# Kernel optimization log

Measured on AMD Instinct MI355X. Metric: run time of the kernel, lower is better.

## Reference

```python
import jax, jax.numpy as jnp
import numpy as np

N = 30000        # nodes
E = 480000       # edges (before self-loops)
F_IN = 512       # input feature dim
HID = 64         # per-head hidden dim
HEADS = 4
WIDTH = HID * HEADS  # 256, concat heads
LAYERS = 3
NCLS = 40
NEG_SLOPE = 0.2


def setup_inputs() -> dict:
    key = jax.random.key(0)
    ks = jax.random.split(key, 16)
    def p(k, shape, scale=0.1):
        return jax.random.normal(k, shape, dtype=jnp.float32) * scale
    return {
        "x": jax.random.normal(ks[0], (N, F_IN), dtype=jnp.float32),
        "edge_index": jax.random.randint(ks[1], (2, E), 0, N, dtype=jnp.int32),
        # layer 1: F_IN -> HEADS*HID (concat)
        "W1": p(ks[2], (F_IN, WIDTH)), "as1": p(ks[3], (HEADS, HID)), "ad1": p(ks[4], (HEADS, HID)), "b1": p(ks[5], (WIDTH,)),
        # layer 2: WIDTH -> WIDTH
        "W2": p(ks[6], (WIDTH, WIDTH)), "as2": p(ks[7], (HEADS, HID)), "ad2": p(ks[8], (HEADS, HID)), "b2": p(ks[9], (WIDTH,)),
        # layer 3: WIDTH -> WIDTH
        "W3": p(ks[10], (WIDTH, WIDTH)), "as3": p(ks[11], (HEADS, HID)), "ad3": p(ks[12], (HEADS, HID)), "b3": p(ks[13], (WIDTH,)),
        # JK='cat' output head: WIDTH*LAYERS -> NCLS
        "Wo": p(ks[14], (WIDTH * LAYERS, NCLS)), "bo": p(ks[15], (NCLS,)),
    }


def gat_layer(x, Wm, a_src, a_dst, b, src, dst):
    # PyG GATConv (concat=True, eval mode): h = xW reshaped [N,H,C];
    # e_ij = leaky_relu(a_src.h_j + a_dst.h_i) for edge j->i, softmax over dst groups.
    n = x.shape[0]
    H, C = a_src.shape
    h = (x @ Wm).reshape(n, H, C)                      # [N,H,C]
    es = jnp.sum(h * a_src, axis=-1)                   # [N,H]
    ed = jnp.sum(h * a_dst, axis=-1)                   # [N,H]
    e = jax.nn.leaky_relu(es[src] + ed[dst], NEG_SLOPE)  # [Etot,H]
    m = jax.ops.segment_max(e, dst, num_segments=n)    # stable softmax per dst node
    w = jnp.exp(e - m[dst])
    den = jax.ops.segment_sum(w, dst, num_segments=n)
    alpha = w / den[dst]                               # [Etot,H]
    out = jax.ops.segment_sum(h[src] * alpha[:, :, None], dst, num_segments=n)  # [N,H,C]
    return out.reshape(n, H * C) + b


def reference(x, edge_index, W1, as1, ad1, b1, W2, as2, ad2, b2, W3, as3, ad3, b3, Wo, bo):
    # add self-loops (PyG GATConv default)
    loops = jnp.arange(N, dtype=edge_index.dtype)
    src = jnp.concatenate([edge_index[0], loops])
    dst = jnp.concatenate([edge_index[1], loops])
    # dropout is identity in eval mode
    h1 = jax.nn.relu(gat_layer(x, W1, as1, ad1, b1, src, dst))
    h2 = jax.nn.relu(gat_layer(h1, W2, as2, ad2, b2, src, dst))
    h3 = jax.nn.relu(gat_layer(h2, W3, as3, ad3, b3, src, dst))
    h = jnp.concatenate([h1, h2, h3], axis=-1)         # JK 'cat': [N, WIDTH*LAYERS]
    return h @ Wo + bo                                 # [N, NCLS]
```

## Files before the change

### kernel.cpp

```cpp
#include <hip/hip_runtime.h>

#define N_NODES 30000
#define N_EDGES 480000
#define ETOT    510000
#define F_IN    512
#define WIDTH   256
#define NCLS    40
#define KCAT    768
#define NPAD    48

typedef __attribute__((ext_vector_type(8))) short short8;
typedef __attribute__((ext_vector_type(4))) float f32x4;

__device__ __forceinline__ unsigned short f2bf(float f){
  unsigned u = __float_as_uint(f);
  u += 0x7fffu + ((u >> 16) & 1u);
  return (unsigned short)(u >> 16);
}
__device__ __forceinline__ float b2f(unsigned short s){
  return __uint_as_float(((unsigned)s) << 16);
}

__global__ void cast4_kernel(const float* __restrict__ in, unsigned short* __restrict__ out, int n4){
  int i = blockIdx.x * blockDim.x + threadIdx.x;
  if (i < n4){
    float4 v = *(const float4*)(in + 4*(size_t)i);
    ushort4 o;
    o.x = f2bf(v.x); o.y = f2bf(v.y); o.z = f2bf(v.z); o.w = f2bf(v.w);
    *(ushort4*)(out + 4*(size_t)i) = o;
  }
}

__global__ void transpose_w_kernel(const float* __restrict__ W, unsigned short* __restrict__ Wt,
                                   int K, int Nc){
  int k = blockIdx.x * blockDim.x + threadIdx.x;
  int n = blockIdx.y;
  if (k < K) Wt[(size_t)n * K + k] = f2bf(W[(size_t)k * Nc + n]);
}

__global__ void transpose_wo_kernel(const float* __restrict__ Wo, unsigned short* __restrict__ WoT){
  int i = blockIdx.x * blockDim.x + threadIdx.x;
  if (i < NPAD * KCAT){
    int c = i / KCAT, k = i - c * KCAT;
    WoT[i] = (c < NCLS) ? f2bf(Wo[(size_t)k * NCLS + c]) : (unsigned short)0;
  }
}

__global__ void zero_kernel(int* __restrict__ p, int n){
  int i = blockIdx.x * blockDim.x + threadIdx.x;
  if (i < n) p[i] = 0;
}

__global__ void hist_kernel(const int* __restrict__ ei, int* __restrict__ counts){
  int e = blockIdx.x * blockDim.x + threadIdx.x;
  if (e < ETOT){
    int d = (e < N_EDGES) ? ei[N_EDGES + e] : (e - N_EDGES);
    atomicAdd(&counts[d], 1);
  }
}

__global__ __launch_bounds__(1024) void scan_kernel(const int* __restrict__ counts,
                                                    int* __restrict__ offsets,
                                                    int* __restrict__ cursor, int n){
  __shared__ int wsum[16];
  int tid = threadIdx.x, lane = tid & 63, wid = tid >> 6;
  int running = 0;
  int nchunks = (n + 1023) >> 10;
  for (int ch = 0; ch < nchunks; ++ch){
    int i = (ch << 10) + tid;
    int v = (i < n) ? counts[i] : 0;
    int x = v;
    #pragma unroll
    for (int off = 1; off < 64; off <<= 1){
      int t = __shfl_up(x, off, 64);
      if (lane >= off) x += t;
    }
    if (lane == 63) wsum[wid] = x;
    __syncthreads();
    if (wid == 0){
      int s = (lane < 16) ? wsum[lane] : 0;
      #pragma unroll
      for (int off = 1; off < 16; off <<= 1){
        int t = __shfl_up(s, off, 64);
        if (lane >= off) s += t;
      }
      if (lane < 16) wsum[lane] = s;
    }
    __syncthreads();
    int waveprefix = (wid > 0) ? wsum[wid - 1] : 0;
    int excl = x - v + waveprefix + running;
    if (i < n){ offsets[i] = excl; cursor[i] = excl; }
    running += wsum[15];
    __syncthreads();
  }
  if (tid == 0) offsets[n] = running;
}

__global__ void scatter_kernel(const int* __restrict__ ei, int* __restrict__ cursor,
                               int* __restrict__ srcs){
  int e = blockIdx.x * blockDim.x + threadIdx.x;
  if (e < ETOT){
    int s, d;
    if (e < N_EDGES){ s = ei[e]; d = ei[N_EDGES + e]; }
    else { s = e - N_EDGES; d = s; }
    int pos = atomicAdd(&cursor[d], 1);
    srcs[pos] = s;
  }
}

#define BM 64
#define BK 32
#define LDA 40

__global__ __launch_bounds__(256) void gemm_bf16_kernel(const unsigned short* __restrict__ A,
                                                        const unsigned short* __restrict__ Bt,
                                                        float* __restrict__ C,
                                                        int M, int K){
  __shared__ unsigned short Als[BM * LDA];
  __shared__ unsigned short Bls[256 * LDA];
  int tid = threadIdx.x;
  int lane = tid & 63, wid = tid >> 6;
  int l15 = lane & 15, quad = lane >> 4;
  int m0 = blockIdx.x * BM;

  f32x4 acc[16];
  #pragma unroll
  for (int t = 0; t < 16; ++t) acc[t] = (f32x4){0.f, 0.f, 0.f, 0.f};

  for (int k0 = 0; k0 < K; k0 += BK){
    __syncthreads();
    {
      int row = tid >> 2, g = tid & 3;
      int grow = m0 + row; if (grow >= M) grow = M - 1;
      uint4 av = *(const uint4*)(A + (size_t)grow * K + k0 + 8 * g);
      *(uint4*)(&Als[row * LDA + 8 * g]) = av;
      const unsigned short* src = Bt + (size_t)tid * K + k0;
      uint4 b0 = *(const uint4*)(src);
      uint4 b1 = *(const uint4*)(src + 8);
      uint4 b2 = *(const uint4*)(src + 16);
      uint4 b3 = *(const uint4*)(src + 24);
      unsigned short* dst = &Bls[tid * LDA];
      *(uint4*)(dst) = b0;
      *(uint4*)(dst + 8) = b1;
      *(uint4*)(dst + 16) = b2;
      *(uint4*)(dst + 24) = b3;
    }
    __syncthreads();
    short8 af = *(const short8*)(&Als[(16 * wid + l15) * LDA + quad * 8]);
    #pragma unroll
    for (int t = 0; t < 16; ++t){
      short8 bf = *(const short8*)(&Bls[(16 * t + l15) * LDA + quad * 8]);
      acc[t] = __builtin_amdgcn_mfma_f32_16x16x32_bf16(af, bf, acc[t], 0, 0, 0);
    }
  }

  int row0 = m0 + 16 * wid + quad * 4;
  #pragma unroll
  for (int t = 0; t < 16; ++t){
    int col = 16 * t + l15;
    #pragma unroll
    for (int r = 0; r < 4; ++r){
      int grow = row0 + r;
      if (grow < M) C[(size_t)grow * WIDTH + col] = acc[t][r];
    }
  }
}

__global__ __launch_bounds__(256) void esed_kernel(const float* __restrict__ hpre,
                                                   const float* __restrict__ a_s,
                                                   const float* __restrict__ a_d,
                                                   float* __restrict__ es, float* __restrict__ ed,
                                                   unsigned short* __restrict__ hb){
  int n = blockIdx.x * 4 + (threadIdx.x >> 6);
  int lane = threadIdx.x & 63;
  float4 h = *(const float4*)(hpre + (size_t)n * WIDTH + 4 * lane);
  int head = lane >> 4, cl = (lane & 15) * 4;
  float4 as = *(const float4*)(a_s + head * 64 + cl);
  float4 ad = *(const float4*)(a_d + head * 64 + cl);
  float ps = h.x * as.x + h.y * as.y + h.z * as.z + h.w * as.w;
  float pd = h.x * ad.x + h.y * ad.y + h.z * ad.z + h.w * ad.w;
  #pragma unroll
  for (int off = 1; off < 16; off <<= 1){
    ps += __shfl_xor(ps, off, 64);
    pd += __shfl_xor(pd, off, 64);
  }
  if ((lane & 15) == 0){
    es[n * 4 + head] = ps;
    ed[n * 4 + head] = pd;
  }
  ushort4 o;
  o.x = f2bf(h.x); o.y = f2bf(h.y); o.z = f2bf(h.z); o.w = f2bf(h.w);
  *(ushort4*)(hb + (size_t)n * WIDTH + 4 * lane) = o;
}

__global__ __launch_bounds__(256) void agg_kernel(const int* __restrict__ offsets,
                                                  const int* __restrict__ srcs,
                                                  const float* __restrict__ es,
                                                  const float* __restrict__ ed,
                                                  const unsigned short* __restrict__ hb,
                                                  const float* __restrict__ bias,
                                                  unsigned short* __restrict__ hout){
  __shared__ float eLds[4][64][4];
  int wid = threadIdx.x >> 6;
  int n = blockIdx.x * 4 + wid;
  int lane = threadIdx.x & 63;
  int half = lane >> 5, l32 = lane & 31;
  int base = offsets[n];
  int deg = offsets[n + 1] - base;
  float4 edv = *(const float4*)(ed + n * 4);

  float m0 = -1e30f, m1 = -1e30f, m2 = -1e30f, m3 = -1e30f;
  for (int i = lane; i < deg; i += 64){
    int s = srcs[base + i];
    float4 ev = *(const float4*)(es + s * 4);
    float e0 = ev.x + edv.x, e1 = ev.y + edv.y, e2 = ev.z + edv.z, e3 = ev.w + edv.w;
    e0 = e0 > 0.f ? e0 : 0.2f * e0;
    e1 = e1 > 0.f ? e1 : 0.2f * e1;
    e2 = e2 > 0.f ? e2 : 0.2f * e2;
    e3 = e3 > 0.f ? e3 : 0.2f * e3;
    if (i < 64) *(float4*)(&eLds[wid][i][0]) = (float4){e0, e1, e2, e3};
    m0 = fmaxf(m0, e0); m1 = fmaxf(m1, e1); m2 = fmaxf(m2, e2); m3 = fmaxf(m3, e3);
  }
  #pragma unroll
  for (int off = 32; off; off >>= 1){
    m0 = fmaxf(m0, __shfl_xor(m0, off, 64));
    m1 = fmaxf(m1, __shfl_xor(m1, off, 64));
    m2 = fmaxf(m2, __shfl_xor(m2, off, 64));
    m3 = fmaxf(m3, __shfl_xor(m3, off, 64));
  }
  int head = l32 >> 3;
  float mh  = (head == 0) ? m0 : (head == 1) ? m1 : (head == 2) ? m2 : m3;
  float edh = (head == 0) ? edv.x : (head == 1) ? edv.y : (head == 2) ? edv.z : edv.w;

  float a0=0.f,a1=0.f,a2=0.f,a3=0.f,a4=0.f,a5=0.f,a6=0.f,a7=0.f;
  float den = 0.f;
  const unsigned short* hcol = hb + 8 * l32;
  for (int i = 0; i < deg; i += 8){
    int sidx[4]; float w[4];
    #pragma unroll
    for (int u = 0; u < 4; ++u){
      int idx = i + 2 * u + half;
      bool v = idx < deg;
      sidx[u] = srcs[base + (v ? idx : 0)];
      float le;
      if (idx < 64){
        le = eLds[wid][v ? idx : 0][head];
      } else {
        float e = es[sidx[u] * 4 + head] + edh;
        le = e > 0.f ? e : 0.2f * e;
      }
      w[u] = v ? __expf(le - mh) : 0.f;
    }
    uint4 hv[4];
    #pragma unroll
    for (int u = 0; u < 4; ++u)
      hv[u] = *(const uint4*)(hcol + (size_t)sidx[u] * WIDTH);
    #pragma unroll
    for (int u = 0; u < 4; ++u){
      float wu = w[u];
      den += wu;
      a0 += wu * b2f((unsigned short)(hv[u].x & 0xffff));
      a1 += wu * b2f((unsigned short)(hv[u].x >> 16));
      a2 += wu * b2f((unsigned short)(hv[u].y & 0xffff));
      a3 += wu * b2f((unsigned short)(hv[u].y >> 16));
      a4 += wu * b2f((unsigned short)(hv[u].z & 0xffff));
      a5 += wu * b2f((unsigned short)(hv[u].z >> 16));
      a6 += wu * b2f((unsigned short)(hv[u].w & 0xffff));
      a7 += wu * b2f((unsigned short)(hv[u].w >> 16));
    }
  }
  den += __shfl_xor(den, 32, 64);
  a0 += __shfl_xor(a0, 32, 64); a1 += __shfl_xor(a1, 32, 64);
  a2 += __shfl_xor(a2, 32, 64); a3 += __shfl_xor(a3, 32, 64);
  a4 += __shfl_xor(a4, 32, 64); a5 += __shfl_xor(a5, 32, 64);
  a6 += __shfl_xor(a6, 32, 64); a7 += __shfl_xor(a7, 32, 64);

  if (half == 0){
    float inv = 1.0f / den;
    const float* bp = bias + 8 * l32;
    float4 bv0 = *(const float4*)(bp);
    float4 bv1 = *(const float4*)(bp + 4);
    float o0 = fmaxf(a0 * inv + bv0.x, 0.f);
    float o1 = fmaxf(a1 * inv + bv0.y, 0.f);
    float o2 = fmaxf(a2 * inv + bv0.z, 0.f);
    float o3 = fmaxf(a3 * inv + bv0.w, 0.f);
    float o4 = fmaxf(a4 * inv + bv1.x, 0.f);
    float o5 = fmaxf(a5 * inv + bv1.y, 0.f);
    float o6 = fmaxf(a6 * inv + bv1.z, 0.f);
    float o7 = fmaxf(a7 * inv + bv1.w, 0.f);
    uint4 o;
    o.x = (unsigned)f2bf(o0) | ((unsigned)f2bf(o1) << 16);
    o.y = (unsigned)f2bf(o2) | ((unsigned)f2bf(o3) << 16);
    o.z = (unsigned)f2bf(o4) | ((unsigned)f2bf(o5) << 16);
    o.w = (unsigned)f2bf(o6) | ((unsigned)f2bf(o7) << 16);
    *(uint4*)(hout + (size_t)n * WIDTH + 8 * l32) = o;
  }
}

__global__ __launch_bounds__(256) void out_gemm_kernel(const unsigned short* __restrict__ h1,
                                                       const unsigned short* __restrict__ h2,
                                                       const unsigned short* __restrict__ h3,
                                                       const unsigned short* __restrict__ WoT,
                                                       const float* __restrict__ bo,
                                                       float* __restrict__ out){
  int tid = threadIdx.x, lane = tid & 63, wid = tid >> 6;
  int l15 = lane & 15, quad = lane >> 4;
  int m0 = blockIdx.x * 64 + 16 * wid;

  f32x4 acc[3];
  #pragma unroll
  for (int t = 0; t < 3; ++t) acc[t] = (f32x4){0.f, 0.f, 0.f, 0.f};

  int arow = m0 + l15; if (arow >= N_NODES) arow = N_NODES - 1;

  #pragma unroll
  for (int part = 0; part < 3; ++part){
    const unsigned short* hp = (part == 0) ? h1 : (part == 1) ? h2 : h3;
    const unsigned short* ap = hp + (size_t)arow * WIDTH;
    #pragma unroll
    for (int k0 = 0; k0 < WIDTH; k0 += 32){
      short8 af = *(const short8*)(ap + k0 + quad * 8);
      int kk = part * WIDTH + k0;
      #pragma unroll
      for (int t = 0; t < 3; ++t){
        short8 bf = *(const short8*)(WoT + (size_t)(16 * t + l15) * KCAT + kk + quad * 8);
        acc[t] = __builtin_amdgcn_mfma_f32_16x16x32_bf16(af, bf, acc[t], 0, 0, 0);
      }
    }
  }

  int r0 = m0 + quad * 4;
  #pragma unroll
  for (int t = 0; t < 3; ++t){
    int col = 16 * t + l15;
    if (col < NCLS){
      float bc = bo[col];
      #pragma unroll
      for (int r = 0; r < 4; ++r){
        int grow = r0 + r;
        if (grow < N_NODES) out[(size_t)grow * NCLS + col] = acc[t][r] + bc;
      }
    }
  }
}

static inline size_t align256(size_t x){ return (x + 255) & ~(size_t)255; }

extern "C" void kernel_launch(void* const* d_in, const int* in_sizes, int n_in,
                              void* d_out, int out_size, void* d_ws, size_t ws_size,
                              hipStream_t stream) {
  const float* x   = (const float*)d_in[0];
  const int*   ei  = (const int*)  d_in[1];
  const float* W1  = (const float*)d_in[2];
  const float* as1 = (const float*)d_in[3];
  const float* ad1 = (const float*)d_in[4];
  const float* b1  = (const float*)d_in[5];
  const float* W2  = (const float*)d_in[6];
  const float* as2 = (const float*)d_in[7];
  const float* ad2 = (const float*)d_in[8];
  const float* b2  = (const float*)d_in[9];
  const float* W3  = (const float*)d_in[10];
  const float* as3 = (const float*)d_in[11];
  const float* ad3 = (const float*)d_in[12];
  const float* b3  = (const float*)d_in[13];
  const float* Wo  = (const float*)d_in[14];
  const float* bo  = (const float*)d_in[15];
  float* out = (float*)d_out;

  char* p = (char*)d_ws;
  auto take = [&](size_t bytes) -> char* { char* cur = p; p += align256(bytes); return cur; };

  unsigned short* xb    = (unsigned short*)take((size_t)N_NODES * F_IN * 2);
  unsigned short* Wt1   = (unsigned short*)take((size_t)WIDTH * F_IN * 2);
  unsigned short* Wt2   = (unsigned short*)take((size_t)WIDTH * WIDTH * 2);
  unsigned short* Wt3   = (unsigned short*)take((size_t)WIDTH * WIDTH * 2);
  unsigned short* WoT   = (unsigned short*)take((size_t)NPAD * KCAT * 2);
  float*          hpre  = (float*)take((size_t)N_NODES * WIDTH * 4);
  unsigned short* hpreb = (unsigned short*)take((size_t)N_NODES * WIDTH * 2);
  float*          es    = (float*)take((size_t)N_NODES * 4 * 4);
  float*          ed    = (float*)take((size_t)N_NODES * 4 * 4);
  unsigned short* h1b   = (unsigned short*)take((size_t)N_NODES * WIDTH * 2);
  unsigned short* h2b   = (unsigned short*)take((size_t)N_NODES * WIDTH * 2);
  unsigned short* h3b   = (unsigned short*)take((size_t)N_NODES * WIDTH * 2);
  int*            counts  = (int*)take((size_t)N_NODES * 4);
  int*            offsets = (int*)take((size_t)(N_NODES + 1) * 4);
  int*            cursor  = (int*)take((size_t)N_NODES * 4);
  int*            srcs    = (int*)take((size_t)ETOT * 4);

  cast4_kernel<<<(N_NODES * F_IN / 4 + 255) / 256, 256, 0, stream>>>(x, xb, N_NODES * F_IN / 4);
  transpose_w_kernel<<<dim3(F_IN / 256, WIDTH), 256, 0, stream>>>(W1, Wt1, F_IN, WIDTH);
  transpose_w_kernel<<<dim3(1, WIDTH), 256, 0, stream>>>(W2, Wt2, WIDTH, WIDTH);
  transpose_w_kernel<<<dim3(1, WIDTH), 256, 0, stream>>>(W3, Wt3, WIDTH, WIDTH);
  transpose_wo_kernel<<<(NPAD * KCAT + 255) / 256, 256, 0, stream>>>(Wo, WoT);

  zero_kernel<<<(N_NODES + 255) / 256, 256, 0, stream>>>(counts, N_NODES);
  hist_kernel<<<(ETOT + 255) / 256, 256, 0, stream>>>(ei, counts);
  scan_kernel<<<1, 1024, 0, stream>>>(counts, offsets, cursor, N_NODES);
  scatter_kernel<<<(ETOT + 255) / 256, 256, 0, stream>>>(ei, cursor, srcs);

  const int gemm_grid = (N_NODES + BM - 1) / BM;
  const int node_grid = N_NODES / 4;

  gemm_bf16_kernel<<<gemm_grid, 256, 0, stream>>>(xb, Wt1, hpre, N_NODES, F_IN);
  esed_kernel<<<node_grid, 256, 0, stream>>>(hpre, as1, ad1, es, ed, hpreb);
  agg_kernel<<<node_grid, 256, 0, stream>>>(offsets, srcs, es, ed, hpreb, b1, h1b);
  gemm_bf16_kernel<<<gemm_grid, 256, 0, stream>>>(h1b, Wt2, hpre, N_NODES, WIDTH);
  esed_kernel<<<node_grid, 256, 0, stream>>>(hpre, as2, ad2, es, ed, hpreb);
  agg_kernel<<<node_grid, 256, 0, stream>>>(offsets, srcs, es, ed, hpreb, b2, h2b);
  gemm_bf16_kernel<<<gemm_grid, 256, 0, stream>>>(h2b, Wt3, hpre, N_NODES, WIDTH);
  esed_kernel<<<node_grid, 256, 0, stream>>>(hpre, as3, ad3, es, ed, hpreb);
  agg_kernel<<<node_grid, 256, 0, stream>>>(offsets, srcs, es, ed, hpreb, b3, h3b);

  out_gemm_kernel<<<gemm_grid, 256, 0, stream>>>(h1b, h2b, h3b, WoT, bo, out);
}
```

Measured before the change: 435.5 us.

## Fuse cast and attention-score epilogue into GEMM; one node per half-wave in aggregation

The layer-1 GEMM now reads fp32 x and converts it to bf16 while loading tiles, which removes the separate cast kernel and the bf16 copy of x. Each GEMM epilogue writes bf16 h directly and computes the es/ed attention dot products from the accumulators with shuffles, which removes the fp32 hpre buffer and the esed kernel. The aggregation kernel assigns one node per 32-lane half-wave instead of splitting a node across two halves, caches source indices in LDS, and unrolls the gather to 8 edges. The trade-off is an extra cross-lane reduction in the GEMM epilogue, plus less parallelism per high-degree node and more register pressure in the aggregation loop.

```diff
diff --git a/kernel.cpp b/kernel.cpp
--- a/kernel.cpp
+++ b/kernel.cpp
@@ -19,16 +19,6 @@
 }
 __device__ __forceinline__ float b2f(unsigned short s){
   return __uint_as_float(((unsigned)s) << 16);
-}
-
-__global__ void cast4_kernel(const float* __restrict__ in, unsigned short* __restrict__ out, int n4){
-  int i = blockIdx.x * blockDim.x + threadIdx.x;
-  if (i < n4){
-    float4 v = *(const float4*)(in + 4*(size_t)i);
-    ushort4 o;
-    o.x = f2bf(v.x); o.y = f2bf(v.y); o.z = f2bf(v.z); o.w = f2bf(v.w);
-    *(ushort4*)(out + 4*(size_t)i) = o;
-  }
 }
 
 __global__ void transpose_w_kernel(const float* __restrict__ W, unsigned short* __restrict__ Wt,
@@ -112,10 +102,15 @@
 #define BK 32
 #define LDA 40
 
-__global__ __launch_bounds__(256) void gemm_bf16_kernel(const unsigned short* __restrict__ A,
-                                                        const unsigned short* __restrict__ Bt,
-                                                        float* __restrict__ C,
-                                                        int M, int K){
+template<bool AF32>
+__global__ __launch_bounds__(256) void gemm_fused_kernel(const void* __restrict__ Araw,
+                                                         const unsigned short* __restrict__ Bt,
+                                                         const float* __restrict__ a_s,
+                                                         const float* __restrict__ a_d,
+                                                         float* __restrict__ es,
+                                                         float* __restrict__ ed,
+                                                         unsigned short* __restrict__ hb,
+                                                         int M, int K){
   __shared__ unsigned short Als[BM * LDA];
   __shared__ unsigned short Bls[256 * LDA];
   int tid = threadIdx.x;
@@ -132,8 +127,19 @@
     {
       int row = tid >> 2, g = tid & 3;
       int grow = m0 + row; if (grow >= M) grow = M - 1;
-      uint4 av = *(const uint4*)(A + (size_t)grow * K + k0 + 8 * g);
-      *(uint4*)(&Als[row * LDA + 8 * g]) = av;
+      if (AF32){
+        const float* Af = (const float*)Araw + (size_t)grow * K + k0 + 8 * g;
+        float4 v0 = *(const float4*)(Af);
+        float4 v1 = *(const float4*)(Af + 4);
+        ushort4 p0 = {f2bf(v0.x), f2bf(v0.y), f2bf(v0.z), f2bf(v0.w)};
+        ushort4 p1 = {f2bf(v1.x), f2bf(v1.y), f2bf(v1.z), f2bf(v1.w)};
+        *(ushort4*)(&Als[row * LDA + 8 * g])     = p0;
+        *(ushort4*)(&Als[row * LDA + 8 * g + 4]) = p1;
+      } else {
+        const unsigned short* Ab = (const unsigned short*)Araw;
+        uint4 av = *(const uint4*)(Ab + (size_t)grow * K + k0 + 8 * g);
+        *(uint4*)(&Als[row * LDA + 8 * g]) = av;
+      }
       const unsigned short* src = Bt + (size_t)tid * K + k0;
       uint4 b0 = *(const uint4*)(src);
       uint4 b1 = *(const uint4*)(src + 8);
@@ -155,42 +161,47 @@
   }
 
   int row0 = m0 + 16 * wid + quad * 4;
+
   #pragma unroll
   for (int t = 0; t < 16; ++t){
     int col = 16 * t + l15;
     #pragma unroll
     for (int r = 0; r < 4; ++r){
       int grow = row0 + r;
-      if (grow < M) C[(size_t)grow * WIDTH + col] = acc[t][r];
-    }
-  }
-}
-
-__global__ __launch_bounds__(256) void esed_kernel(const float* __restrict__ hpre,
-                                                   const float* __restrict__ a_s,
-                                                   const float* __restrict__ a_d,
-                                                   float* __restrict__ es, float* __restrict__ ed,
-                                                   unsigned short* __restrict__ hb){
-  int n = blockIdx.x * 4 + (threadIdx.x >> 6);
-  int lane = threadIdx.x & 63;
-  float4 h = *(const float4*)(hpre + (size_t)n * WIDTH + 4 * lane);
-  int head = lane >> 4, cl = (lane & 15) * 4;
-  float4 as = *(const float4*)(a_s + head * 64 + cl);
-  float4 ad = *(const float4*)(a_d + head * 64 + cl);
-  float ps = h.x * as.x + h.y * as.y + h.z * as.z + h.w * as.w;
-  float pd = h.x * ad.x + h.y * ad.y + h.z * ad.z + h.w * ad.w;
-  #pragma unroll
-  for (int off = 1; off < 16; off <<= 1){
-    ps += __shfl_xor(ps, off, 64);
-    pd += __shfl_xor(pd, off, 64);
-  }
-  if ((lane & 15) == 0){
-    es[n * 4 + head] = ps;
-    ed[n * 4 + head] = pd;
-  }
-  ushort4 o;
-  o.x = f2bf(h.x); o.y = f2bf(h.y); o.z = f2bf(h.z); o.w = f2bf(h.w);
-  *(ushort4*)(hb + (size_t)n * WIDTH + 4 * lane) = o;
+      if (grow < M) hb[(size_t)grow * WIDTH + col] = f2bf(acc[t][r]);
+    }
+  }
+
+  float as_v[16], ad_v[16];
+  #pragma unroll
+  for (int t = 0; t < 16; ++t){
+    int cc = 16 * (t & 3) + l15;
+    as_v[t] = a_s[(t >> 2) * 64 + cc];
+    ad_v[t] = a_d[(t >> 2) * 64 + cc];
+  }
+  #pragma unroll
+  for (int h = 0; h < 4; ++h){
+    #pragma unroll
+    for (int r = 0; r < 4; ++r){
+      float se = 0.f, sd = 0.f;
+      #pragma unroll
+      for (int tt = 0; tt < 4; ++tt){
+        int t = 4 * h + tt;
+        se += acc[t][r] * as_v[t];
+        sd += acc[t][r] * ad_v[t];
+      }
+      #pragma unroll
+      for (int off = 1; off < 16; off <<= 1){
+        se += __shfl_xor(se, off, 64);
+        sd += __shfl_xor(sd, off, 64);
+      }
+      int grow = row0 + r;
+      if (l15 == 0 && grow < M){
+        es[grow * 4 + h] = se;
+        ed[grow * 4 + h] = sd;
+      }
+    }
+  }
 }
 
 __global__ __launch_bounds__(256) void agg_kernel(const int* __restrict__ offsets,
@@ -200,17 +211,19 @@
                                                   const unsigned short* __restrict__ hb,
                                                   const float* __restrict__ bias,
                                                   unsigned short* __restrict__ hout){
-  __shared__ float eLds[4][64][4];
+  __shared__ float eLds[8][64][4];
+  __shared__ int   sLds[8][64];
   int wid = threadIdx.x >> 6;
-  int n = blockIdx.x * 4 + wid;
   int lane = threadIdx.x & 63;
   int half = lane >> 5, l32 = lane & 31;
+  int slot = wid * 2 + half;
+  int n = blockIdx.x * 8 + slot;
   int base = offsets[n];
   int deg = offsets[n + 1] - base;
   float4 edv = *(const float4*)(ed + n * 4);
 
   float m0 = -1e30f, m1 = -1e30f, m2 = -1e30f, m3 = -1e30f;
-  for (int i = lane; i < deg; i += 64){
+  for (int i = l32; i < deg; i += 32){
     int s = srcs[base + i];
     float4 ev = *(const float4*)(es + s * 4);
     float e0 = ev.x + edv.x, e1 = ev.y + edv.y, e2 = ev.z + edv.z, e3 = ev.w + edv.w;
@@ -218,11 +231,14 @@
     e1 = e1 > 0.f ? e1 : 0.2f * e1;
     e2 = e2 > 0.f ? e2 : 0.2f * e2;
     e3 = e3 > 0.f ? e3 : 0.2f * e3;
-    if (i < 64) *(float4*)(&eLds[wid][i][0]) = (float4){e0, e1, e2, e3};
+    if (i < 64){
+      sLds[slot][i] = s;
+      *(float4*)(&eLds[slot][i][0]) = (float4){e0, e1, e2, e3};
+    }
     m0 = fmaxf(m0, e0); m1 = fmaxf(m1, e1); m2 = fmaxf(m2, e2); m3 = fmaxf(m3, e3);
   }
   #pragma unroll
-  for (int off = 32; off; off >>= 1){
+  for (int off = 1; off < 32; off <<= 1){
     m0 = fmaxf(m0, __shfl_xor(m0, off, 64));
     m1 = fmaxf(m1, __shfl_xor(m1, off, 64));
     m2 = fmaxf(m2, __shfl_xor(m2, off, 64));
@@ -232,69 +248,65 @@
   float mh  = (head == 0) ? m0 : (head == 1) ? m1 : (head == 2) ? m2 : m3;
   float edh = (head == 0) ? edv.x : (head == 1) ? edv.y : (head == 2) ? edv.z : edv.w;
 
-  float a0=0.f,a1=0.f,a2=0.f,a3=0.f,a4=0.f,a5=0.f,a6=0.f,a7=0.f;
+  float2 a0 = {0.f,0.f}, a1 = {0.f,0.f}, a2 = {0.f,0.f}, a3 = {0.f,0.f};
   float den = 0.f;
   const unsigned short* hcol = hb + 8 * l32;
   for (int i = 0; i < deg; i += 8){
-    int sidx[4]; float w[4];
-    #pragma unroll
-    for (int u = 0; u < 4; ++u){
-      int idx = i + 2 * u + half;
+    int sidx[8]; float w[8];
+    #pragma unroll
+    for (int u = 0; u < 8; ++u){
+      int idx = i + u;
       bool v = idx < deg;
-      sidx[u] = srcs[base + (v ? idx : 0)];
-      float le;
-      if (idx < 64){
-        le = eLds[wid][v ? idx : 0][head];
+      float le; int s;
+      if (idx < 64 || !v){
+        int ic = v ? idx : 0;
+        if (ic >= 64) ic = 0;
+        s  = sLds[slot][ic];
+        le = eLds[slot][ic][head];
       } else {
-        float e = es[sidx[u] * 4 + head] + edh;
+        s = srcs[base + idx];
+        float e = es[s * 4 + head] + edh;
         le = e > 0.f ? e : 0.2f * e;
       }
+      sidx[u] = s;
       w[u] = v ? __expf(le - mh) : 0.f;
     }
-    uint4 hv[4];
-    #pragma unroll
-    for (int u = 0; u < 4; ++u)
+    uint4 hv[8];
+    #pragma unroll
+    for (int u = 0; u < 8; ++u)
       hv[u] = *(const uint4*)(hcol + (size_t)sidx[u] * WIDTH);
     #pragma unroll
-    for (int u = 0; u < 4; ++u){
+    for (int u = 0; u < 8; ++u){
       float wu = w[u];
       den += wu;
-      a0 += wu * b2f((unsigned short)(hv[u].x & 0xffff));
-      a1 += wu * b2f((unsigned short)(hv[u].x >> 16));
-      a2 += wu * b2f((unsigned short)(hv[u].y & 0xffff));
-      a3 += wu * b2f((unsigned short)(hv[u].y >> 16));
-      a4 += wu * b2f((unsigned short)(hv[u].z & 0xffff));
-      a5 += wu * b2f((unsigned short)(hv[u].z >> 16));
-      a6 += wu * b2f((unsigned short)(hv[u].w & 0xffff));
-      a7 += wu * b2f((unsigned short)(hv[u].w >> 16));
-    }
-  }
-  den += __shfl_xor(den, 32, 64);
-  a0 += __shfl_xor(a0, 32, 64); a1 += __shfl_xor(a1, 32, 64);
-  a2 += __shfl_xor(a2, 32, 64); a3 += __shfl_xor(a3, 32, 64);
-  a4 += __shfl_xor(a4, 32, 64); a5 += __shfl_xor(a5, 32, 64);
-  a6 += __shfl_xor(a6, 32, 64); a7 += __shfl_xor(a7, 32, 64);
-
-  if (half == 0){
-    float inv = 1.0f / den;
-    const float* bp = bias + 8 * l32;
-    float4 bv0 = *(const float4*)(bp);
-    float4 bv1 = *(const float4*)(bp + 4);
-    float o0 = fmaxf(a0 * inv + bv0.x, 0.f);
-    float o1 = fmaxf(a1 * inv + bv0.y, 0.f);
-    float o2 = fmaxf(a2 * inv + bv0.z, 0.f);
-    float o3 = fmaxf(a3 * inv + bv0.w, 0.f);
-    float o4 = fmaxf(a4 * inv + bv1.x, 0.f);
-    float o5 = fmaxf(a5 * inv + bv1.y, 0.f);
-    float o6 = fmaxf(a6 * inv + bv1.z, 0.f);
-    float o7 = fmaxf(a7 * inv + bv1.w, 0.f);
-    uint4 o;
-    o.x = (unsigned)f2bf(o0) | ((unsigned)f2bf(o1) << 16);
-    o.y = (unsigned)f2bf(o2) | ((unsigned)f2bf(o3) << 16);
-    o.z = (unsigned)f2bf(o4) | ((unsigned)f2bf(o5) << 16);
-    o.w = (unsigned)f2bf(o6) | ((unsigned)f2bf(o7) << 16);
-    *(uint4*)(hout + (size_t)n * WIDTH + 8 * l32) = o;
-  }
+      a0.x += wu * __uint_as_float(hv[u].x << 16);
+      a0.y += wu * __uint_as_float(hv[u].x & 0xffff0000u);
+      a1.x += wu * __uint_as_float(hv[u].y << 16);
+      a1.y += wu * __uint_as_float(hv[u].y & 0xffff0000u);
+      a2.x += wu * __uint_as_float(hv[u].z << 16);
+      a2.y += wu * __uint_as_float(hv[u].z & 0xffff0000u);
+      a3.x += wu * __uint_as_float(hv[u].w << 16);
+      a3.y += wu * __uint_as_float(hv[u].w & 0xffff0000u);
+    }
+  }
+  float inv = 1.0f / den;
+  const float* bp = bias + 8 * l32;
+  float4 bv0 = *(const float4*)(bp);
+  float4 bv1 = *(const float4*)(bp + 4);
+  float o0 = fmaxf(a0.x * inv + bv0.x, 0.f);
+  float o1 = fmaxf(a0.y * inv + bv0.y, 0.f);
+  float o2 = fmaxf(a1.x * inv + bv0.z, 0.f);
+  float o3 = fmaxf(a1.y * inv + bv0.w, 0.f);
+  float o4 = fmaxf(a2.x * inv + bv1.x, 0.f);
+  float o5 = fmaxf(a2.y * inv + bv1.y, 0.f);
+  float o6 = fmaxf(a3.x * inv + bv1.z, 0.f);
+  float o7 = fmaxf(a3.y * inv + bv1.w, 0.f);
+  uint4 o;
+  o.x = (unsigned)f2bf(o0) | ((unsigned)f2bf(o1) << 16);
+  o.y = (unsigned)f2bf(o2) | ((unsigned)f2bf(o3) << 16);
+  o.z = (unsigned)f2bf(o4) | ((unsigned)f2bf(o5) << 16);
+  o.w = (unsigned)f2bf(o6) | ((unsigned)f2bf(o7) << 16);
+  *(uint4*)(hout + (size_t)n * WIDTH + 8 * l32) = o;
 }
 
 __global__ __launch_bounds__(256) void out_gemm_kernel(const unsigned short* __restrict__ h1,
@@ -370,13 +382,11 @@
   char* p = (char*)d_ws;
   auto take = [&](size_t bytes) -> char* { char* cur = p; p += align256(bytes); return cur; };
 
-  unsigned short* xb    = (unsigned short*)take((size_t)N_NODES * F_IN * 2);
   unsigned short* Wt1   = (unsigned short*)take((size_t)WIDTH * F_IN * 2);
   unsigned short* Wt2   = (unsigned short*)take((size_t)WIDTH * WIDTH * 2);
   unsigned short* Wt3   = (unsigned short*)take((size_t)WIDTH * WIDTH * 2);
   unsigned short* WoT   = (unsigned short*)take((size_t)NPAD * KCAT * 2);
-  float*          hpre  = (float*)take((size_t)N_NODES * WIDTH * 4);
-  unsigned short* hpreb = (unsigned short*)take((size_t)N_NODES * WIDTH * 2);
+  unsigned short* hstage= (unsigned short*)take((size_t)N_NODES * WIDTH * 2);
   float*          es    = (float*)take((size_t)N_NODES * 4 * 4);
   float*          ed    = (float*)take((size_t)N_NODES * 4 * 4);
   unsigned short* h1b   = (unsigned short*)take((size_t)N_NODES * WIDTH * 2);
@@ -387,7 +397,6 @@
   int*            cursor  = (int*)take((size_t)N_NODES * 4);
   int*            srcs    = (int*)take((size_t)ETOT * 4);
 
-  cast4_kernel<<<(N_NODES * F_IN / 4 + 255) / 256, 256, 0, stream>>>(x, xb, N_NODES * F_IN / 4);
   transpose_w_kernel<<<dim3(F_IN / 256, WIDTH), 256, 0, stream>>>(W1, Wt1, F_IN, WIDTH);
   transpose_w_kernel<<<dim3(1, WIDTH), 256, 0, stream>>>(W2, Wt2, WIDTH, WIDTH);
   transpose_w_kernel<<<dim3(1, WIDTH), 256, 0, stream>>>(W3, Wt3, WIDTH, WIDTH);
@@ -399,17 +408,14 @@
   scatter_kernel<<<(ETOT + 255) / 256, 256, 0, stream>>>(ei, cursor, srcs);
 
   const int gemm_grid = (N_NODES + BM - 1) / BM;
-  const int node_grid = N_NODES / 4;
-
-  gemm_bf16_kernel<<<gemm_grid, 256, 0, stream>>>(xb, Wt1, hpre, N_NODES, F_IN);
-  esed_kernel<<<node_grid, 256, 0, stream>>>(hpre, as1, ad1, es, ed, hpreb);
-  agg_kernel<<<node_grid, 256, 0, stream>>>(offsets, srcs, es, ed, hpreb, b1, h1b);
-  gemm_bf16_kernel<<<gemm_grid, 256, 0, stream>>>(h1b, Wt2, hpre, N_NODES, WIDTH);
-  esed_kernel<<<node_grid, 256, 0, stream>>>(hpre, as2, ad2, es, ed, hpreb);
-  agg_kernel<<<node_grid, 256, 0, stream>>>(offsets, srcs, es, ed, hpreb, b2, h2b);
-  gemm_bf16_kernel<<<gemm_grid, 256, 0, stream>>>(h2b, Wt3, hpre, N_NODES, WIDTH);
-  esed_kernel<<<node_grid, 256, 0, stream>>>(hpre, as3, ad3, es, ed, hpreb);
-  agg_kernel<<<node_grid, 256, 0, stream>>>(offsets, srcs, es, ed, hpreb, b3, h3b);
+  const int agg_grid  = N_NODES / 8;
+
+  gemm_fused_kernel<true><<<gemm_grid, 256, 0, stream>>>(x, Wt1, as1, ad1, es, ed, hstage, N_NODES, F_IN);
+  agg_kernel<<<agg_grid, 256, 0, stream>>>(offsets, srcs, es, ed, hstage, b1, h1b);
+  gemm_fused_kernel<false><<<gemm_grid, 256, 0, stream>>>(h1b, Wt2, as2, ad2, es, ed, hstage, N_NODES, WIDTH);
+  agg_kernel<<<agg_grid, 256, 0, stream>>>(offsets, srcs, es, ed, hstage, b2, h2b);
+  gemm_fused_kernel<false><<<gemm_grid, 256, 0, stream>>>(h2b, Wt3, as3, ad3, es, ed, hstage, N_NODES, WIDTH);
+  agg_kernel<<<agg_grid, 256, 0, stream>>>(offsets, srcs, es, ed, hstage, b3, h3b);
 
   out_gemm_kernel<<<gemm_grid, 256, 0, stream>>>(h1b, h2b, h3b, WoT, bo, out);
 }
```

New measurement: 411.6 us. -5.5%, faster.
